# Kernel optimization log

Measured on AMD Instinct MI355X. Metric: run time of the kernel, lower is better.

The kernel has to match this reference:

```python
import jax, jax.numpy as jnp
import numpy as np

N, E = 50000, 800000
IN, HID, OUT, H, REL, RD = 768, 256, 128, 8, 6, 64


def setup_inputs() -> dict:
    key = jax.random.key(0)
    ks = jax.random.split(key, 16)
    g = lambda i, shape, sc: jax.random.normal(ks[i], shape, jnp.float32) * sc
    return dict(
        x=g(0, (N, IN), 1.0),
        edge_index=jax.random.randint(ks[1], (2, E), 0, N),
        edge_type=jax.random.randint(ks[2], (E,), 0, REL),
        rel_emb=g(3, (REL, RD), 0.1),
        W1=g(4, (IN, HID), 0.03),
        att_src1=g(5, (H, HID // H), 0.1),
        att_dst1=g(6, (H, HID // H), 0.1),
        We1=g(7, (RD, HID), 0.1),
        att_e1=g(8, (H, HID // H), 0.1),
        b1=jnp.zeros((HID,), jnp.float32),
        g1=jnp.ones((HID,), jnp.float32),
        beta1=jnp.zeros((HID,), jnp.float32),
        W2=g(9, (HID, OUT), 0.06),
        att_src2=g(10, (1, OUT), 0.1),
        att_dst2=g(11, (1, OUT), 0.1),
        b2=jnp.zeros((OUT,), jnp.float32),
        g2=jnp.ones((OUT,), jnp.float32),
        beta2=jnp.zeros((OUT,), jnp.float32),
    )


def _gat(x, src, dst, W, a_s, a_d, bias, heads, ch, e_feat=None, We=None, a_e=None):
    # PyG GATConv (shared lin, concat=True, negative_slope=0.2, eval-mode dropout)
    n = x.shape[0]
    h = (x @ W).reshape(n, heads, ch)              # [N,H,C]
    al_s = (h * a_s).sum(-1)                       # [N,H]
    al_d = (h * a_d).sum(-1)
    alpha = al_s[src] + al_d[dst]                  # [Etot,H]
    if e_feat is not None:
        e = (e_feat @ We).reshape(-1, heads, ch)
        alpha = alpha + (e * a_e).sum(-1)
    alpha = jax.nn.leaky_relu(alpha, 0.2)
    mx = jax.ops.segment_max(alpha, dst, num_segments=n)   # segment softmax over dst
    ex = jnp.exp(alpha - mx[dst])
    den = jax.ops.segment_sum(ex, dst, num_segments=n)
    w = ex / (den[dst] + 1e-16)
    out = jax.ops.segment_sum(h[src] * w[:, :, None], dst, num_segments=n)
    return out.reshape(n, heads * ch) + bias


def _ln(x, g, b):
    m = x.mean(-1, keepdims=True)
    v = x.var(-1, keepdims=True)
    return (x - m) / jnp.sqrt(v + 1e-5) * g + b


def reference(x, edge_index, edge_type, rel_emb, W1, att_src1, att_dst1, We1, att_e1,
              b1, g1, beta1, W2, att_src2, att_dst2, b2, g2, beta2):
    n = x.shape[0]
    src0, dst0 = edge_index[0], edge_index[1]
    loop = jnp.arange(n)
    src = jnp.concatenate([src0, loop])
    dst = jnp.concatenate([dst0, loop])
    rel_feat = rel_emb[edge_type]                   # [E,RD]
    # self-loop edge_attr = mean of incoming edge_attr (fill_value='mean')
    cnt = jax.ops.segment_sum(jnp.ones((src0.shape[0],), jnp.float32), dst0, num_segments=n)
    self_attr = jax.ops.segment_sum(rel_feat, dst0, num_segments=n) / jnp.maximum(cnt, 1.0)[:, None]
    e_feat = jnp.concatenate([rel_feat, self_attr], 0)
    h = _gat(x, src, dst, W1, att_src1, att_dst1, b1, H, HID // H, e_feat, We1, att_e1)
    h = jax.nn.elu(_ln(h, g1, beta1))
    h = _gat(h, src, dst, W2, att_src2, att_dst2, b2, 1, OUT)
    return _ln(h, g2, beta2)
```

## Files before the change

### kernel.cpp

```cpp
#include <hip/hip_runtime.h>
#include <hip/hip_bf16.h>

#define IN_DIM 768
#define HID 256
#define OUT_DIM 128
#define NHEAD 8
#define NREL 6
#define RD 64

typedef unsigned short ushort_t;
typedef float f32x4 __attribute__((ext_vector_type(4)));
typedef __bf16 bf16x8 __attribute__((ext_vector_type(8)));
typedef unsigned short u16x8 __attribute__((ext_vector_type(8)));
typedef unsigned short u16x4 __attribute__((ext_vector_type(4)));
typedef unsigned short u16x2 __attribute__((ext_vector_type(2)));

typedef const __attribute__((address_space(1))) void* gptr_t;
typedef __attribute__((address_space(3))) void* lptr_t;

static __device__ __forceinline__ float leaky(float x) { return x > 0.f ? x : 0.2f * x; }

static __device__ __forceinline__ ushort_t f2bf(float f) {
    union { __hip_bfloat16 h; ushort_t u; } c;
    c.h = __float2bfloat16(f);
    return c.u;
}

static __device__ __forceinline__ float b2f(ushort_t u) {
    union { unsigned int i; float f; } c;
    c.i = ((unsigned int)u) << 16;
    return c.f;
}

__global__ void count_kernel(const int* __restrict__ dst0, int* __restrict__ deg, int E) {
    int e = blockIdx.x * blockDim.x + threadIdx.x;
    if (e >= E) return;
    atomicAdd(&deg[dst0[e]], 1);
}

__global__ void __launch_bounds__(256) scanA(const int* __restrict__ deg,
                                             int* __restrict__ bsum, int n) {
    __shared__ int sh[4];
    int b = blockIdx.x, t = threadIdx.x;
    int s = 0;
#pragma unroll
    for (int j = 0; j < 4; j++) {
        int idx = b * 1024 + t * 4 + j;
        if (idx < n) s += deg[idx];
    }
    for (int o = 32; o > 0; o >>= 1) s += __shfl_xor(s, o, 64);
    if ((t & 63) == 0) sh[t >> 6] = s;
    __syncthreads();
    if (t == 0) bsum[b] = sh[0] + sh[1] + sh[2] + sh[3];
}

__global__ void __launch_bounds__(256) scanB(const int* __restrict__ bsum,
                                             int* __restrict__ bbase,
                                             int* __restrict__ rowptr, int nb, int n) {
    __shared__ int sh[256];
    int t = threadIdx.x;
    int v = (t < nb) ? bsum[t] : 0;
    sh[t] = v;
    __syncthreads();
    for (int o = 1; o < 256; o <<= 1) {
        int add = (t >= o) ? sh[t - o] : 0;
        __syncthreads();
        sh[t] += add;
        __syncthreads();
    }
    if (t < nb) bbase[t] = sh[t] - v;
    if (t == 255) rowptr[n] = sh[255];
}

__global__ void __launch_bounds__(256) scanC(const int* __restrict__ deg,
                                             const int* __restrict__ bbase,
                                             int* __restrict__ rowptr, int n) {
    __shared__ int sh[256];
    int b = blockIdx.x, t = threadIdx.x;
    int base = b * 1024;
    int loc[4];
    int run = 0;
#pragma unroll
    for (int j = 0; j < 4; j++) {
        int idx = base + t * 4 + j;
        int d = (idx < n) ? deg[idx] : 0;
        loc[j] = run;
        run += d;
    }
    int tot = run;
    sh[t] = run;
    __syncthreads();
    for (int o = 1; o < 256; o <<= 1) {
        int add = (t >= o) ? sh[t - o] : 0;
        __syncthreads();
        sh[t] += add;
        __syncthreads();
    }
    int texcl = sh[t] - tot;
    int bb = bbase[b];
#pragma unroll
    for (int j = 0; j < 4; j++) {
        int idx = base + t * 4 + j;
        if (idx < n) rowptr[idx] = bb + texcl + loc[j];
    }
}

__global__ void scatter_kernel(const int* __restrict__ src0, const int* __restrict__ dst0,
                               const int* __restrict__ ety, const int* __restrict__ rowptr,
                               int* __restrict__ fill, int* __restrict__ src_pk, int E) {
    int e = blockIdx.x * blockDim.x + threadIdx.x;
    if (e >= E) return;
    int d = dst0[e];
    int pos = rowptr[d] + atomicAdd(&fill[d], 1);
    src_pk[pos] = src0[e] | (ety[e] << 24);
}

__global__ void rel_alpha_kernel(const float* __restrict__ rel_emb, const float* __restrict__ We1,
                                 const float* __restrict__ att_e1, float* __restrict__ rel_alpha) {
    int t = threadIdx.x;
    if (t >= NREL * NHEAD) return;
    int r = t / NHEAD, h = t % NHEAD;
    float acc = 0.f;
    for (int c = 0; c < HID / NHEAD; c++) {
        float v = 0.f;
        for (int k = 0; k < RD; k++) v += rel_emb[r * RD + k] * We1[k * HID + h * 32 + c];
        acc += v * att_e1[h * 32 + c];
    }
    rel_alpha[r * NHEAD + h] = acc;
}

__global__ void prep_weights(const float* __restrict__ W1, const float* __restrict__ W2,
                             ushort_t* __restrict__ W1t, ushort_t* __restrict__ W2t) {
    int i = blockIdx.x * 256 + threadIdx.x;
    if (i < IN_DIM * HID) {
        int k = i / HID, n = i % HID;
        W1t[n * IN_DIM + k] = f2bf(W1[i]);
    } else {
        int j = i - IN_DIM * HID;
        if (j < HID * OUT_DIM) {
            int k = j / OUT_DIM, n = j % OUT_DIM;
            W2t[n * HID + k] = f2bf(W2[j]);
        }
    }
}

__global__ void __launch_bounds__(512) gemm_f32a(const float* __restrict__ Af,
                                                 const ushort_t* __restrict__ Bt,
                                                 ushort_t* __restrict__ C,
                                                 int K,
                                                 const float* __restrict__ att_s,
                                                 const float* __restrict__ att_d,
                                                 float* __restrict__ als,
                                                 float* __restrict__ ald, int N) {
    __shared__ float sAf[128 * 64];
    __shared__ ushort_t sB[256 * 64];
    const int Nout = 256;
    int T = gridDim.x;
    int p = blockIdx.x;
    int q8 = T >> 3, rr8 = T & 7, xc = p & 7, jj0 = p >> 3;
    int l = (xc < rr8 ? xc * (q8 + 1) : rr8 * (q8 + 1) + (xc - rr8) * q8) + jj0;
    int m0 = l * 128;
    int t = threadIdx.x;
    int w = t >> 6, ln = t & 63;
    int wm = (w >> 2) * 64, wn = (w & 3) * 64;

    const float* agp[4];
#pragma unroll
    for (int i = 0; i < 4; i++) {
        int rl = w * 16 + i * 4 + (ln >> 4);
        int rg = min(m0 + rl, N - 1);
        int cc = (ln & 15) ^ (rl & 15);
        agp[i] = Af + (size_t)rg * K + (cc << 2);
    }
    const ushort_t* bgp[4];
#pragma unroll
    for (int i = 0; i < 4; i++) {
        int rl = w * 32 + i * 8 + (ln >> 3);
        int cc = (ln & 7) ^ (ln >> 3);
        bgp[i] = Bt + (size_t)rl * K + (cc << 3);
    }

    f32x4 acc[4][4] = {};

    for (int k0 = 0; k0 < K; k0 += 64) {
#pragma unroll
        for (int i = 0; i < 4; i++)
            __builtin_amdgcn_global_load_lds((gptr_t)(const void*)(agp[i] + k0),
                                             (lptr_t)(void*)(&sAf[(w * 16 + i * 4) * 64]),
                                             16, 0, 0);
#pragma unroll
        for (int i = 0; i < 4; i++)
            __builtin_amdgcn_global_load_lds((gptr_t)(const void*)(bgp[i] + k0),
                                             (lptr_t)(void*)(&sB[(w * 32 + i * 8) * 64]),
                                             16, 0, 0);
        __syncthreads();
#pragma unroll
        for (int ks = 0; ks < 2; ks++) {
            bf16x8 af[4], bfr[4];
#pragma unroll
            for (int m = 0; m < 4; m++) {
                int r = wm + m * 16 + (ln & 15);
                int key = r & 15;
                int c0 = ks * 8 + (ln >> 4) * 2;
                const f32x4* rowp = reinterpret_cast<const f32x4*>(&sAf[r * 64]);
                f32x4 lo = rowp[c0 ^ key];
                f32x4 hi = rowp[(c0 + 1) ^ key];
                union { u16x8 u; bf16x8 b; } cv;
                cv.u[0] = f2bf(lo[0]); cv.u[1] = f2bf(lo[1]);
                cv.u[2] = f2bf(lo[2]); cv.u[3] = f2bf(lo[3]);
                cv.u[4] = f2bf(hi[0]); cv.u[5] = f2bf(hi[1]);
                cv.u[6] = f2bf(hi[2]); cv.u[7] = f2bf(hi[3]);
                af[m] = cv.b;
            }
#pragma unroll
            for (int n = 0; n < 4; n++) {
                int r = wn + n * 16 + (ln & 15);
                int key = r & 7;
                int cB = ks * 4 + (ln >> 4);
                bfr[n] = *reinterpret_cast<const bf16x8*>(&sB[r * 64 + ((cB ^ key) << 3)]);
            }
#pragma unroll
            for (int m = 0; m < 4; m++)
#pragma unroll
                for (int n = 0; n < 4; n++)
                    acc[m][n] = __builtin_amdgcn_mfma_f32_16x16x32_bf16(af[m], bfr[n], acc[m][n], 0, 0, 0);
        }
        __syncthreads();
    }

    int cc = ln & 15, qq = ln >> 4;
#pragma unroll
    for (int m = 0; m < 4; m++) {
#pragma unroll
        for (int rr = 0; rr < 4; rr++) {
            int row = m0 + wm + m * 16 + qq * 4 + rr;
#pragma unroll
            for (int n = 0; n < 4; n++)
                C[(size_t)row * Nout + wn + n * 16 + cc] = f2bf(acc[m][n][rr]);
        }
    }

    float as_[4], ad_[4];
#pragma unroll
    for (int n = 0; n < 4; n++) {
        int col = wn + n * 16 + cc;
        as_[n] = att_s[col];
        ad_[n] = att_d[col];
    }
    int hbase = wn >> 5;
#pragma unroll
    for (int m = 0; m < 4; m++) {
#pragma unroll
        for (int rr = 0; rr < 4; rr++) {
            int row = m0 + wm + m * 16 + qq * 4 + rr;
            float ps0 = acc[m][0][rr] * as_[0] + acc[m][1][rr] * as_[1];
            float ps1 = acc[m][2][rr] * as_[2] + acc[m][3][rr] * as_[3];
            float pd0 = acc[m][0][rr] * ad_[0] + acc[m][1][rr] * ad_[1];
            float pd1 = acc[m][2][rr] * ad_[2] + acc[m][3][rr] * ad_[3];
#pragma unroll
            for (int o = 1; o < 16; o <<= 1) {
                ps0 += __shfl_xor(ps0, o, 64);
                ps1 += __shfl_xor(ps1, o, 64);
                pd0 += __shfl_xor(pd0, o, 64);
                pd1 += __shfl_xor(pd1, o, 64);
            }
            if (cc == 0 && row < N) {
                als[row * NHEAD + hbase] = ps0;
                als[row * NHEAD + hbase + 1] = ps1;
                ald[row * NHEAD + hbase] = pd0;
                ald[row * NHEAD + hbase + 1] = pd1;
            }
        }
    }
}

__global__ void __launch_bounds__(256) gemm_lds2(const ushort_t* __restrict__ A,
                                                 const ushort_t* __restrict__ Bt,
                                                 ushort_t* __restrict__ C,
                                                 int K, int Nout, int NBlk,
                                                 const float* __restrict__ att_s,
                                                 const float* __restrict__ att_d,
                                                 float* __restrict__ als,
                                                 float* __restrict__ ald, int N) {
    __shared__ ushort_t sA[2][128 * 32];
    __shared__ ushort_t sB[2][128 * 32];
    int T = gridDim.x;
    int p = blockIdx.x;
    int q8 = T >> 3, rr8 = T & 7, xc = p & 7, j = p >> 3;
    int l = (xc < rr8 ? xc * (q8 + 1) : rr8 * (q8 + 1) + (xc - rr8) * q8) + j;
    int m0 = (l / NBlk) * 128;
    int n0 = (l % NBlk) * 128;
    int t = threadIdx.x;
    int w = t >> 6, ln = t & 63;
    int wm = (w >> 1) * 64, wn = (w & 1) * 64;

    const ushort_t* ag = A + (size_t)(m0 + w * 32 + (ln >> 2)) * K + (ln & 3) * 8;
    const ushort_t* bg = Bt + (size_t)(n0 + w * 32 + (ln >> 2)) * K + (ln & 3) * 8;

    f32x4 acc[4][4] = {};

    auto stage = [&](int buf, int k0) {
#pragma unroll
        for (int i = 0; i < 2; i++) {
            __builtin_amdgcn_global_load_lds(
                (gptr_t)(const void*)(ag + (size_t)i * 16 * K + k0),
                (lptr_t)(void*)(&sA[buf][(w * 32 + i * 16) * 32]), 16, 0, 0);
            __builtin_amdgcn_global_load_lds(
                (gptr_t)(const void*)(bg + (size_t)i * 16 * K + k0),
                (lptr_t)(void*)(&sB[buf][(w * 32 + i * 16) * 32]), 16, 0, 0);
        }
    };

    int nt = K >> 5;
    stage(0, 0);
    __syncthreads();
    int cur = 0;
    for (int tt = 0; tt < nt; tt++) {
        if (tt + 1 < nt) stage(cur ^ 1, (tt + 1) << 5);
        bf16x8 af[4], bfr[4];
#pragma unroll
        for (int m = 0; m < 4; m++)
            af[m] = *reinterpret_cast<const bf16x8*>(
                &sA[cur][(wm + m * 16 + (ln & 15)) * 32 + (ln >> 4) * 8]);
#pragma unroll
        for (int n = 0; n < 4; n++)
            bfr[n] = *reinterpret_cast<const bf16x8*>(
                &sB[cur][(wn + n * 16 + (ln & 15)) * 32 + (ln >> 4) * 8]);
#pragma unroll
        for (int m = 0; m < 4; m++)
#pragma unroll
            for (int n = 0; n < 4; n++)
                acc[m][n] = __builtin_amdgcn_mfma_f32_16x16x32_bf16(af[m], bfr[n], acc[m][n], 0, 0, 0);
        __syncthreads();
        cur ^= 1;
    }

    int cc = ln & 15, qq = ln >> 4;
#pragma unroll
    for (int m = 0; m < 4; m++) {
#pragma unroll
        for (int rr = 0; rr < 4; rr++) {
            int row = m0 + wm + m * 16 + qq * 4 + rr;
#pragma unroll
            for (int n = 0; n < 4; n++)
                C[(size_t)row * Nout + n0 + wn + n * 16 + cc] = f2bf(acc[m][n][rr]);
        }
    }

    float as_[4], ad_[4];
#pragma unroll
    for (int n = 0; n < 4; n++) {
        int col = n0 + wn + n * 16 + cc;
        as_[n] = att_s[col];
        ad_[n] = att_d[col];
    }
    __shared__ float sh_s[2][128];
    __shared__ float sh_d[2][128];
#pragma unroll
    for (int m = 0; m < 4; m++) {
#pragma unroll
        for (int rr = 0; rr < 4; rr++) {
            int rib = wm + m * 16 + qq * 4 + rr;
            float ps = acc[m][0][rr] * as_[0] + acc[m][1][rr] * as_[1] +
                       acc[m][2][rr] * as_[2] + acc[m][3][rr] * as_[3];
            float pd = acc[m][0][rr] * ad_[0] + acc[m][1][rr] * ad_[1] +
                       acc[m][2][rr] * ad_[2] + acc[m][3][rr] * ad_[3];
#pragma unroll
            for (int o = 1; o < 16; o <<= 1) {
                ps += __shfl_xor(ps, o, 64);
                pd += __shfl_xor(pd, o, 64);
            }
            if (cc == 0) {
                sh_s[wn >> 6][rib] = ps;
                sh_d[wn >> 6][rib] = pd;
            }
        }
    }
    __syncthreads();
    if (t < 128) {
        int row = m0 + t;
        if (row < N) {
            als[row] = sh_s[0][t] + sh_s[1][t];
            ald[row] = sh_d[0][t] + sh_d[1][t];
        }
    }
}

__global__ void __launch_bounds__(256) node_agg1(
    const ushort_t* __restrict__ h1b, const float* __restrict__ als, const float* __restrict__ ald,
    const float* __restrict__ rel_alpha, const int* __restrict__ rowptr,
    const int* __restrict__ src_pk,
    const float* __restrict__ b1, const float* __restrict__ g1, const float* __restrict__ beta1,
    ushort_t* __restrict__ out, int N) {
    __shared__ float sh_rel[NREL * NHEAD];
    if (threadIdx.x < NREL * NHEAD) sh_rel[threadIdx.x] = rel_alpha[threadIdx.x];
    __syncthreads();
    int l = threadIdx.x & 63;
    int i = blockIdx.x * 4 + (threadIdx.x >> 6);
    if (i >= N) return;
    int h = l & 7;
    int e8 = l >> 3;
    float als_i = als[i * NHEAD + h];
    float ald_h = ald[i * NHEAD + h];
    float c0, c1, c2, c3;
    {
        u16x4 v = *reinterpret_cast<const u16x4*>(h1b + (size_t)i * HID + 4 * l);
        c0 = b2f(v[0]); c1 = b2f(v[1]); c2 = b2f(v[2]); c3 = b2f(v[3]);
    }
    int base = rowptr[i];
    int deg = rowptr[i + 1] - base;
    const char* hb = reinterpret_cast<const char*>(h1b);
    float acc0 = 0.f, acc1 = 0.f, acc2 = 0.f, acc3 = 0.f;
    float csum = 0.f, rs = 0.f;
    for (int cs = 0; cs < deg; cs += 8) {
        int c = min(8, deg - cs);
        float w = 0.f, ra = 0.f;
        unsigned offv = 0;
        if (e8 < c) {
            int pk = src_pk[base + cs + e8];
            int sv = pk & 0xFFFFFF;
            int tv = (unsigned)pk >> 24;
            ra = sh_rel[tv * NHEAD + h];
            w = __expf(fminf(leaky(als[sv * NHEAD + h] + ald_h + ra), 40.f));
            offv = (unsigned)sv * (HID * 2);
        }
        csum += w;
        rs += ra;
        if (c == 8) {
            float wt[8];
            unsigned of[8];
            u16x4 v[8];
#pragma unroll
            for (int e = 0; e < 8; e++) {
                wt[e] = __shfl(w, e * 8 + e8, 64);
                of[e] = (unsigned)__shfl((int)offv, e * 8, 64);
            }
#pragma unroll
            for (int e = 0; e < 8; e++)
                v[e] = *reinterpret_cast<const u16x4*>(hb + of[e] + 8 * l);
#pragma unroll
            for (int e = 0; e < 8; e++) {
                acc0 += wt[e] * b2f(v[e][0]);
                acc1 += wt[e] * b2f(v[e][1]);
                acc2 += wt[e] * b2f(v[e][2]);
                acc3 += wt[e] * b2f(v[e][3]);
            }
        } else {
            for (int e = 0; e < c; e++) {
                float wt = __shfl(w, e * 8 + e8, 64);
                unsigned of = (unsigned)__shfl((int)offv, e * 8, 64);
                u16x4 v = *reinterpret_cast<const u16x4*>(hb + of + 8 * l);
                acc0 += wt * b2f(v[0]); acc1 += wt * b2f(v[1]);
                acc2 += wt * b2f(v[2]); acc3 += wt * b2f(v[3]);
            }
        }
    }
    for (int o = 8; o < 64; o <<= 1) {
        csum += __shfl_xor(csum, o, 64);
        rs += __shfl_xor(rs, o, 64);
    }
    float selfa = rs / fmaxf((float)deg, 1.0f);
    float wself = __expf(fminf(leaky(als_i + ald_h + selfa), 40.f));
    float stot = csum + wself;
    float s_g = __shfl(stot, e8, 64);
    float w_g = __shfl(wself, e8, 64);
    acc0 += w_g * c0; acc1 += w_g * c1; acc2 += w_g * c2; acc3 += w_g * c3;
    float inv = 1.0f / (s_g + 1e-16f);
    float4 bb = *reinterpret_cast<const float4*>(b1 + 4 * l);
    float y0 = acc0 * inv + bb.x, y1 = acc1 * inv + bb.y;
    float y2 = acc2 * inv + bb.z, y3 = acc3 * inv + bb.w;
    float su = y0 + y1 + y2 + y3;
    float sq = y0 * y0 + y1 * y1 + y2 * y2 + y3 * y3;
    for (int o = 1; o < 64; o <<= 1) {
        su += __shfl_xor(su, o, 64);
        sq += __shfl_xor(sq, o, 64);
    }
    float mean = su * (1.f / 256.f);
    float var = sq * (1.f / 256.f) - mean * mean;
    float rstd = rsqrtf(var + 1e-5f);
    float4 gg = *reinterpret_cast<const float4*>(g1 + 4 * l);
    float4 be = *reinterpret_cast<const float4*>(beta1 + 4 * l);
    float z0 = (y0 - mean) * rstd * gg.x + be.x;
    float z1 = (y1 - mean) * rstd * gg.y + be.y;
    float z2 = (y2 - mean) * rstd * gg.z + be.z;
    float z3 = (y3 - mean) * rstd * gg.w + be.w;
    u16x4 ov;
    ov[0] = f2bf(z0 > 0.f ? z0 : __expf(z0) - 1.f);
    ov[1] = f2bf(z1 > 0.f ? z1 : __expf(z1) - 1.f);
    ov[2] = f2bf(z2 > 0.f ? z2 : __expf(z2) - 1.f);
    ov[3] = f2bf(z3 > 0.f ? z3 : __expf(z3) - 1.f);
    *reinterpret_cast<u16x4*>(out + (size_t)i * HID + 4 * l) = ov;
}

__global__ void __launch_bounds__(256) node_agg2(const ushort_t* __restrict__ h2b,
                                                 const float* __restrict__ als,
                                                 const float* __restrict__ ald,
                                                 const int* __restrict__ rowptr,
                                                 const int* __restrict__ src_pk,
                                                 const float* __restrict__ b2,
                                                 const float* __restrict__ g2,
                                                 const float* __restrict__ beta2,
                                                 float* __restrict__ out, int N) {
    int l = threadIdx.x & 63;
    int i = blockIdx.x * 4 + (threadIdx.x >> 6);
    if (i >= N) return;
    float aldi = ald[i];
    float alsi = als[i];
    float c0, c1;
    {
        u16x2 v = *reinterpret_cast<const u16x2*>(h2b + (size_t)i * OUT_DIM + 2 * l);
        c0 = b2f(v[0]); c1 = b2f(v[1]);
    }
    int base = rowptr[i];
    int deg = rowptr[i + 1] - base;
    const char* hb = reinterpret_cast<const char*>(h2b);
    float acc0 = 0.f, acc1 = 0.f;
    float csum = 0.f;
    for (int cs = 0; cs < deg; cs += 64) {
        int c = min(64, deg - cs);
        float w = 0.f;
        unsigned offv = 0;
        if (l < c) {
            int sv = src_pk[base + cs + l] & 0xFFFFFF;
            w = __expf(fminf(leaky(als[sv] + aldi), 40.f));
            offv = (unsigned)sv * (OUT_DIM * 2);
        }
        csum += w;
        int e = 0;
        for (; e + 8 <= c; e += 8) {
            float wt[8];
            unsigned of[8];
            u16x2 v[8];
#pragma unroll
            for (int jj = 0; jj < 8; jj++) {
                wt[jj] = __shfl(w, e + jj, 64);
                of[jj] = (unsigned)__shfl((int)offv, e + jj, 64);
            }
#pragma unroll
            for (int jj = 0; jj < 8; jj++)
                v[jj] = *reinterpret_cast<const u16x2*>(hb + of[jj] + 4 * l);
#pragma unroll
            for (int jj = 0; jj < 8; jj++) {
                acc0 += wt[jj] * b2f(v[jj][0]);
                acc1 += wt[jj] * b2f(v[jj][1]);
            }
        }
        for (; e < c; e++) {
            float wt = __shfl(w, e, 64);
            unsigned of = (unsigned)__shfl((int)offv, e, 64);
            u16x2 v = *reinterpret_cast<const u16x2*>(hb + of + 4 * l);
            acc0 += wt * b2f(v[0]); acc1 += wt * b2f(v[1]);
        }
    }
    for (int o = 1; o < 64; o <<= 1) csum += __shfl_xor(csum, o, 64);
    float wself = __expf(fminf(leaky(alsi + aldi), 40.f));
    float s = csum + wself;
    acc0 += wself * c0; acc1 += wself * c1;
    float inv = 1.0f / (s + 1e-16f);
    float2 bb = *reinterpret_cast<const float2*>(b2 + 2 * l);
    float y0 = acc0 * inv + bb.x, y1 = acc1 * inv + bb.y;
    float su = y0 + y1, sq = y0 * y0 + y1 * y1;
    for (int o = 1; o < 64; o <<= 1) {
        su += __shfl_xor(su, o, 64);
        sq += __shfl_xor(sq, o, 64);
    }
    float mean = su * (1.f / 128.f);
    float var = sq * (1.f / 128.f) - mean * mean;
    float rstd = rsqrtf(var + 1e-5f);
    float2 gg = *reinterpret_cast<const float2*>(g2 + 2 * l);
    float2 be = *reinterpret_cast<const float2*>(beta2 + 2 * l);
    float2 ov;
    ov.x = (y0 - mean) * rstd * gg.x + be.x;
    ov.y = (y1 - mean) * rstd * gg.y + be.y;
    *reinterpret_cast<float2*>(out + (size_t)i * OUT_DIM + 2 * l) = ov;
}

extern "C" void kernel_launch(void* const* d_in, const int* in_sizes, int n_in,
                              void* d_out, int out_size, void* d_ws, size_t ws_size,
                              hipStream_t stream) {
    const float* x = (const float*)d_in[0];
    const int* ei = (const int*)d_in[1];
    const int* ety = (const int*)d_in[2];
    const float* rel_emb = (const float*)d_in[3];
    const float* W1 = (const float*)d_in[4];
    const float* att_s1 = (const float*)d_in[5];
    const float* att_d1 = (const float*)d_in[6];
    const float* We1 = (const float*)d_in[7];
    const float* att_e1 = (const float*)d_in[8];
    const float* b1 = (const float*)d_in[9];
    const float* g1 = (const float*)d_in[10];
    const float* beta1 = (const float*)d_in[11];
    const float* W2 = (const float*)d_in[12];
    const float* att_s2 = (const float*)d_in[13];
    const float* att_d2 = (const float*)d_in[14];
    const float* b2 = (const float*)d_in[15];
    const float* g2 = (const float*)d_in[16];
    const float* beta2 = (const float*)d_in[17];

    int N = in_sizes[0] / IN_DIM;
    int E = in_sizes[1] / 2;
    int Mpad = ((N + 127) / 128) * 128;
    const int* src0 = ei;
    const int* dst0 = ei + E;

    char* ws = (char*)d_ws;
    size_t off = 0;
    auto alloc = [&](size_t bytes) -> void* {
        off = (off + 255) & ~(size_t)255;
        void* p = ws + off;
        off += bytes;
        return p;
    };
    int* deg = (int*)alloc((size_t)N * 4);
    int* fill = (int*)alloc((size_t)N * 4);
    int* rowptr = (int*)alloc((size_t)(N + 1) * 4);
    int* src_pk = (int*)alloc((size_t)E * 4);
    int nb = (N + 1023) >> 10;
    int* bsum = (int*)alloc((size_t)nb * 4);
    int* bbase = (int*)alloc((size_t)nb * 4);
    float* rel_alpha = (float*)alloc(NREL * NHEAD * 4);
    float* als1 = (float*)alloc((size_t)N * NHEAD * 4);
    float* ald1 = (float*)alloc((size_t)N * NHEAD * 4);
    float* al2s = (float*)alloc((size_t)N * 4);
    float* al2d = (float*)alloc((size_t)N * 4);
    ushort_t* W1t = (ushort_t*)alloc((size_t)HID * IN_DIM * 2);
    ushort_t* W2t = (ushort_t*)alloc((size_t)OUT_DIM * HID * 2);
    ushort_t* h1b = (ushort_t*)alloc((size_t)Mpad * HID * 2);
    ushort_t* h1pb = (ushort_t*)alloc((size_t)Mpad * HID * 2);
    ushort_t* h2b = h1b;

    hipMemsetAsync(deg, 0, (size_t)N * 4, stream);
    hipMemsetAsync(fill, 0, (size_t)N * 4, stream);

    int eb = (E + 255) / 256;
    count_kernel<<<eb, 256, 0, stream>>>(dst0, deg, E);
    scanA<<<nb, 256, 0, stream>>>(deg, bsum, N);
    scanB<<<1, 256, 0, stream>>>(bsum, bbase, rowptr, nb, N);
    scanC<<<nb, 256, 0, stream>>>(deg, bbase, rowptr, N);
    scatter_kernel<<<eb, 256, 0, stream>>>(src0, dst0, ety, rowptr, fill, src_pk, E);
    rel_alpha_kernel<<<1, 64, 0, stream>>>(rel_emb, We1, att_e1, rel_alpha);
    prep_weights<<<(IN_DIM * HID + HID * OUT_DIM + 255) / 256, 256, 0, stream>>>(W1, W2, W1t, W2t);

    int T1 = Mpad / 128;
    gemm_f32a<<<T1, 512, 0, stream>>>(x, W1t, h1b, IN_DIM,
                                      att_s1, att_d1, als1, ald1, N);
    hipMemsetAsync(h1pb + (size_t)N * HID, 0, (size_t)(Mpad - N) * HID * 2, stream);
    node_agg1<<<(N + 3) / 4, 256, 0, stream>>>(h1b, als1, ald1, rel_alpha, rowptr, src_pk,
                                               b1, g1, beta1, h1pb, N);

    int NB2 = OUT_DIM / 128;
    int T2 = (Mpad / 128) * NB2;
    gemm_lds2<<<T2, 256, 0, stream>>>(h1pb, W2t, h2b, HID, OUT_DIM, NB2,
                                      att_s2, att_d2, al2s, al2d, N);
    node_agg2<<<(N + 3) / 4, 256, 0, stream>>>(h2b, al2s, al2d, rowptr, src_pk, b2, g2, beta2,
                                               (float*)d_out, N);
}
```

Measured before the change: 359.7 us.

## Double-buffer layer-1 GEMM LDS tiles with smaller 64-row blocks

The first-layer GEMM moves from 128-row tiles with 512 threads and a single 64-wide K stage to 64-row tiles with 256 threads and two 32-wide K buffers. The next K tile is prefetched with direct-to-LDS loads while the current one is computed, using vmcnt waits and raw barriers in place of full __syncthreads. The aim is to overlap global loads with MFMA work and to raise the block count for better occupancy. In exchange, each B tile is loaded by twice as many blocks, which adds global/L2 traffic for B, and the hand-written waitcnt count is fragile.

```diff
diff --git a/kernel.cpp b/kernel.cpp
--- a/kernel.cpp
+++ b/kernel.cpp
@@ -144,7 +144,7 @@
     }
 }
 
-__global__ void __launch_bounds__(512) gemm_f32a(const float* __restrict__ Af,
+__global__ void __launch_bounds__(256) gemm_f32a(const float* __restrict__ Af,
                                                  const ushort_t* __restrict__ Bt,
                                                  ushort_t* __restrict__ C,
                                                  int K,
@@ -152,59 +152,71 @@
                                                  const float* __restrict__ att_d,
                                                  float* __restrict__ als,
                                                  float* __restrict__ ald, int N) {
-    __shared__ float sAf[128 * 64];
-    __shared__ ushort_t sB[256 * 64];
+    __shared__ float sAf[2][64 * 32];
+    __shared__ ushort_t sB[2][256 * 32];
     const int Nout = 256;
     int T = gridDim.x;
     int p = blockIdx.x;
     int q8 = T >> 3, rr8 = T & 7, xc = p & 7, jj0 = p >> 3;
     int l = (xc < rr8 ? xc * (q8 + 1) : rr8 * (q8 + 1) + (xc - rr8) * q8) + jj0;
-    int m0 = l * 128;
+    int m0 = l * 64;
     int t = threadIdx.x;
     int w = t >> 6, ln = t & 63;
-    int wm = (w >> 2) * 64, wn = (w & 3) * 64;
-
-    const float* agp[4];
+    int wn = w * 64;
+
+    const float* agp[2];
+#pragma unroll
+    for (int i = 0; i < 2; i++) {
+        int rl = w * 16 + i * 8 + (ln >> 3);
+        int rg = min(m0 + rl, N - 1);
+        int cc = (ln & 7) ^ (ln >> 3);
+        agp[i] = Af + (size_t)rg * K + (cc << 2);
+    }
+    const ushort_t* bgp[4];
 #pragma unroll
     for (int i = 0; i < 4; i++) {
-        int rl = w * 16 + i * 4 + (ln >> 4);
-        int rg = min(m0 + rl, N - 1);
-        int cc = (ln & 15) ^ (rl & 15);
-        agp[i] = Af + (size_t)rg * K + (cc << 2);
-    }
-    const ushort_t* bgp[4];
-#pragma unroll
-    for (int i = 0; i < 4; i++) {
-        int rl = w * 32 + i * 8 + (ln >> 3);
-        int cc = (ln & 7) ^ (ln >> 3);
+        int rl = w * 64 + i * 16 + (ln >> 2);
+        int cc = (ln & 3) ^ ((ln >> 3) & 3);
         bgp[i] = Bt + (size_t)rl * K + (cc << 3);
     }
 
     f32x4 acc[4][4] = {};
 
-    for (int k0 = 0; k0 < K; k0 += 64) {
-#pragma unroll
-        for (int i = 0; i < 4; i++)
+    auto stage = [&](int buf, int k0) {
+#pragma unroll
+        for (int i = 0; i < 2; i++)
             __builtin_amdgcn_global_load_lds((gptr_t)(const void*)(agp[i] + k0),
-                                             (lptr_t)(void*)(&sAf[(w * 16 + i * 4) * 64]),
+                                             (lptr_t)(void*)(&sAf[buf][(w * 16 + i * 8) * 32]),
                                              16, 0, 0);
 #pragma unroll
         for (int i = 0; i < 4; i++)
             __builtin_amdgcn_global_load_lds((gptr_t)(const void*)(bgp[i] + k0),
-                                             (lptr_t)(void*)(&sB[(w * 32 + i * 8) * 64]),
+                                             (lptr_t)(void*)(&sB[buf][(w * 64 + i * 16) * 32]),
                                              16, 0, 0);
-        __syncthreads();
-#pragma unroll
-        for (int ks = 0; ks < 2; ks++) {
+    };
+
+    int nt = K >> 5;
+    int cur = 0;
+    stage(0, 0);
+    for (int tt = 0; tt < nt; tt++) {
+        if (tt + 1 < nt) {
+            stage(cur ^ 1, (tt + 1) << 5);
+            asm volatile("s_waitcnt vmcnt(6)" ::: "memory");
+        } else {
+            asm volatile("s_waitcnt vmcnt(0)" ::: "memory");
+        }
+        __builtin_amdgcn_sched_barrier(0);
+        __builtin_amdgcn_s_barrier();
+        {
             bf16x8 af[4], bfr[4];
+            int q = ln >> 4;
 #pragma unroll
             for (int m = 0; m < 4; m++) {
-                int r = wm + m * 16 + (ln & 15);
-                int key = r & 15;
-                int c0 = ks * 8 + (ln >> 4) * 2;
-                const f32x4* rowp = reinterpret_cast<const f32x4*>(&sAf[r * 64]);
-                f32x4 lo = rowp[c0 ^ key];
-                f32x4 hi = rowp[(c0 + 1) ^ key];
+                int r = m * 16 + (ln & 15);
+                int key = r & 7;
+                const f32x4* rowp = reinterpret_cast<const f32x4*>(&sAf[cur][r * 32]);
+                f32x4 lo = rowp[(2 * q) ^ key];
+                f32x4 hi = rowp[(2 * q + 1) ^ key];
                 union { u16x8 u; bf16x8 b; } cv;
                 cv.u[0] = f2bf(lo[0]); cv.u[1] = f2bf(lo[1]);
                 cv.u[2] = f2bf(lo[2]); cv.u[3] = f2bf(lo[3]);
@@ -215,9 +227,8 @@
 #pragma unroll
             for (int n = 0; n < 4; n++) {
                 int r = wn + n * 16 + (ln & 15);
-                int key = r & 7;
-                int cB = ks * 4 + (ln >> 4);
-                bfr[n] = *reinterpret_cast<const bf16x8*>(&sB[r * 64 + ((cB ^ key) << 3)]);
+                int key = (r >> 1) & 3;
+                bfr[n] = *reinterpret_cast<const bf16x8*>(&sB[cur][r * 32 + ((q ^ key) << 3)]);
             }
 #pragma unroll
             for (int m = 0; m < 4; m++)
@@ -225,7 +236,8 @@
                 for (int n = 0; n < 4; n++)
                     acc[m][n] = __builtin_amdgcn_mfma_f32_16x16x32_bf16(af[m], bfr[n], acc[m][n], 0, 0, 0);
         }
-        __syncthreads();
+        __builtin_amdgcn_s_barrier();
+        cur ^= 1;
     }
 
     int cc = ln & 15, qq = ln >> 4;
@@ -233,7 +245,7 @@
     for (int m = 0; m < 4; m++) {
 #pragma unroll
         for (int rr = 0; rr < 4; rr++) {
-            int row = m0 + wm + m * 16 + qq * 4 + rr;
+            int row = m0 + m * 16 + qq * 4 + rr;
 #pragma unroll
             for (int n = 0; n < 4; n++)
                 C[(size_t)row * Nout + wn + n * 16 + cc] = f2bf(acc[m][n][rr]);
@@ -252,7 +264,7 @@
     for (int m = 0; m < 4; m++) {
 #pragma unroll
         for (int rr = 0; rr < 4; rr++) {
-            int row = m0 + wm + m * 16 + qq * 4 + rr;
+            int row = m0 + m * 16 + qq * 4 + rr;
             float ps0 = acc[m][0][rr] * as_[0] + acc[m][1][rr] * as_[1];
             float ps1 = acc[m][2][rr] * as_[2] + acc[m][3][rr] * as_[3];
             float pd0 = acc[m][0][rr] * ad_[0] + acc[m][1][rr] * ad_[1];
@@ -641,8 +653,8 @@
     rel_alpha_kernel<<<1, 64, 0, stream>>>(rel_emb, We1, att_e1, rel_alpha);
     prep_weights<<<(IN_DIM * HID + HID * OUT_DIM + 255) / 256, 256, 0, stream>>>(W1, W2, W1t, W2t);
 
-    int T1 = Mpad / 128;
-    gemm_f32a<<<T1, 512, 0, stream>>>(x, W1t, h1b, IN_DIM,
+    int T1 = Mpad / 64;
+    gemm_f32a<<<T1, 256, 0, stream>>>(x, W1t, h1b, IN_DIM,
                                       att_s1, att_d1, als1, ald1, N);
     hipMemsetAsync(h1pb + (size_t)N * HID, 0, (size_t)(Mpad - N) * HID * 2, stream);
     node_agg1<<<(N + 3) / 4, 256, 0, stream>>>(h1b, als1, ald1, rel_alpha, rowptr, src_pk,
```

After: 350.7 us. -2.5%, faster.
